# Kernel tuning notes

Measured on AMD Instinct MI355X. Metric: run time of the kernel, lower is better.

Reference implementation:

```python
import jax, jax.numpy as jnp
import numpy as np

# Mamba2 config (matches mamba_ssm.Mamba2 defaults used by the wrapper)
D_MODEL = 1024
D_STATE = 128
D_CONV = 4
EXPAND = 2
HEADDIM = 64
CHUNK = 256
D_INNER = EXPAND * D_MODEL            # 2048
NHEADS = D_INNER // HEADDIM           # 32
CONV_DIM = D_INNER + 2 * D_STATE      # 2304 (x, B, C share the causal conv)
D_IN_PROJ = 2 * D_INNER + 2 * D_STATE + NHEADS  # z, xBC, dt
EPS = 1e-5


def rmsnorm(x, w, eps=EPS):
    return x * jax.lax.rsqrt(jnp.mean(x * x, axis=-1, keepdims=True) + eps) * w


def setup_inputs() -> dict:
    key = jax.random.key(0)
    ks = jax.random.split(key, 8)
    B, L = 2, 2048
    def w(k, shape, sc=0.02):
        return jax.random.normal(k, shape, jnp.float32) * sc
    return {
        "x": jax.random.normal(ks[0], (B, L, D_MODEL), jnp.float32),
        "norm_w": jnp.ones((D_MODEL,), jnp.float32),
        "in_proj_w": w(ks[1], (D_IN_PROJ, D_MODEL)),
        "conv_w": w(ks[2], (CONV_DIM, 1, D_CONV), 0.2),   # depthwise kernel
        "conv_b": jnp.zeros((CONV_DIM,), jnp.float32),
        "dt_bias": w(ks[3], (NHEADS,), 1.0),
        "A_log": jnp.log(1.0 + 15.0 * jax.random.uniform(ks[4], (NHEADS,), jnp.float32)),
        "D": jnp.ones((NHEADS,), jnp.float32),
        "gnorm_w": jnp.ones((D_INNER,), jnp.float32),
        "out_proj_w": w(ks[5], (D_MODEL, D_INNER)),
    }


def _ssd(xd, a, Bm, Cm):
    """Chunked SSD scan (ssd_minimal_discrete).
    xd: (b,l,h,p) = x*dt ; a: (b,l,h) = dt*A ; Bm,Cm: (b,l,n) (ngroups=1)."""
    b, l, h, p = xd.shape
    n = Bm.shape[-1]
    nc = l // CHUNK
    xd = xd.reshape(b, nc, CHUNK, h, p)
    a = a.reshape(b, nc, CHUNK, h).transpose(0, 3, 1, 2)   # (b,h,nc,c)
    Bm = Bm.reshape(b, nc, CHUNK, n)
    Cm = Cm.reshape(b, nc, CHUNK, n)
    a_cs = jnp.cumsum(a, axis=-1)                           # (b,h,nc,c)
    # 1) intra-chunk: causal decay matrix L[t,s] = exp(sum_{s<i<=t} a_i)
    diff = a_cs[..., :, None] - a_cs[..., None, :]          # (b,h,nc,c,c)
    mask = jnp.tril(jnp.ones((CHUNK, CHUNK), bool))
    Lm = jnp.exp(jnp.where(mask, diff, 0.0)) * mask
    Y_diag = jnp.einsum("bcln,bcsn,bhcls,bcshp->bclhp", Cm, Bm, Lm, xd)
    # 2) per-chunk end states
    decay_states = jnp.exp(a_cs[..., -1:] - a_cs)           # (b,h,nc,c)
    states = jnp.einsum("bcln,bhcl,bclhp->bchpn", Bm, decay_states, xd)
    # 3) inter-chunk recurrence (vectorized segsum over the 8+1 chunk totals)
    tot = jnp.pad(a_cs[..., -1], ((0, 0), (0, 0), (1, 0)))  # (b,h,nc+1)
    tot_cs = jnp.cumsum(tot, axis=-1)
    dchunk = tot_cs[..., :, None] - tot_cs[..., None, :]    # (b,h,nc+1,nc+1)
    cmask = jnp.tril(jnp.ones((nc + 1, nc + 1), bool))
    dchunk = jnp.exp(jnp.where(cmask, dchunk, 0.0)) * cmask
    states = jnp.concatenate([jnp.zeros_like(states[:, :1]), states], axis=1)
    new_states = jnp.einsum("bhzc,bchpn->bzhpn", dchunk, states)
    init_states = new_states[:, :-1]                        # state entering each chunk
    # 4) state -> output contribution
    Y_off = jnp.einsum("bcln,bchpn,bhcl->bclhp", Cm, init_states, jnp.exp(a_cs))
    return (Y_diag + Y_off).reshape(b, l, h, p)


def reference(x, norm_w, in_proj_w, conv_w, conv_b, dt_bias, A_log, D, gnorm_w, out_proj_w):
    res = x
    u = rmsnorm(x, norm_w)
    zxbcdt = u @ in_proj_w.T                                # (b,l,d_in_proj)
    z, xBC, dt = jnp.split(zxbcdt, [D_INNER, D_INNER + CONV_DIM], axis=-1)
    # causal depthwise conv1d over (x,B,C), then SiLU
    xBC_t = jnp.pad(xBC.transpose(0, 2, 1), ((0, 0), (0, 0), (D_CONV - 1, 0)))
    conv = jax.lax.conv_general_dilated(
        xBC_t, conv_w, (1,), "VALID",
        dimension_numbers=("NCH", "OIH", "NCH"), feature_group_count=CONV_DIM)
    xBC = jax.nn.silu(conv.transpose(0, 2, 1) + conv_b)
    xs, Bm, Cm = jnp.split(xBC, [D_INNER, D_INNER + D_STATE], axis=-1)
    dt = jax.nn.softplus(dt + dt_bias)                      # (b,l,h)
    A = -jnp.exp(A_log)                                     # (h,)
    xh = xs.reshape(xs.shape[0], xs.shape[1], NHEADS, HEADDIM)
    y = _ssd(xh * dt[..., None], dt * A, Bm, Cm)
    y = y + D[None, None, :, None] * xh                     # skip term
    y = y.reshape(xs.shape)
    y = rmsnorm(y * jax.nn.silu(z), gnorm_w)                # gated RMSNorm
    return res + y @ out_proj_w.T
```

## Files before the change

kernel.cpp:

```cpp
#include <hip/hip_runtime.h>
#include <hip/hip_bf16.h>

typedef __hip_bfloat16 bf16_t;
typedef __attribute__((ext_vector_type(8))) short bfrag8;
typedef __attribute__((ext_vector_type(4))) float floatx4;

#define DM     1024
#define DI     2048
#define NHD    32
#define HD     64
#define DSTATE 128
#define CONVD  2304
#define NPROJ  4384
#define NPAD   4480
#define MR     4096
#define LL     2048
#define EPSF   1e-5f
#define LOG2E  1.44269504088896f

__device__ __forceinline__ void gl_lds16(const void* g, void* l) {
  __builtin_amdgcn_global_load_lds((const __attribute__((address_space(1))) void*)g,
                                   (__attribute__((address_space(3))) void*)l, 16, 0, 0);
}
__device__ __forceinline__ unsigned pack_bf16_rn(float a, float b) {
  unsigned ua = (__float_as_uint(a) + 0x8000u) >> 16;
  unsigned ub = (__float_as_uint(b) + 0x8000u) >> 16;
  return ua | (ub << 16);
}
__device__ __forceinline__ unsigned short bf16u(float a) {
  return (unsigned short)((__float_as_uint(a) + 0x8000u) >> 16);
}
__device__ __forceinline__ float blo(unsigned u){ return __uint_as_float(u << 16); }
__device__ __forceinline__ float bhi(unsigned u){ return __uint_as_float(u & 0xffff0000u); }
__device__ __forceinline__ void unp8(uint4 u, float* v) {
  v[0]=blo(u.x); v[1]=bhi(u.x); v[2]=blo(u.y); v[3]=bhi(u.y);
  v[4]=blo(u.z); v[5]=bhi(u.z); v[6]=blo(u.w); v[7]=bhi(u.w);
}
typedef union { unsigned u[4]; bfrag8 f; } fragu;

#define W1CNT (NPAD * DM / 4)
#define W2CNT (DM * DI / 4)
#define CVTBLK ((W1CNT + W2CNT) / 256)
__global__ void rms_cvt_kernel(const float* __restrict__ x, const float* __restrict__ w,
                               bf16_t* __restrict__ ub,
                               const float* __restrict__ w1, const float* __restrict__ w2,
                               const float* __restrict__ gw,
                               bf16_t* __restrict__ o1, bf16_t* __restrict__ o2) {
  __shared__ float red[4];
  int t = threadIdx.x;
  if (blockIdx.x < MR) {
    int row = blockIdx.x;
    float4 v = ((const float4*)(x + (long)row * DM))[t];
    float ss = v.x*v.x + v.y*v.y + v.z*v.z + v.w*v.w;
#pragma unroll
    for (int off = 32; off > 0; off >>= 1) ss += __shfl_down(ss, off, 64);
    if ((t & 63) == 0) red[t >> 6] = ss;
    __syncthreads();
    float tot = red[0] + red[1] + red[2] + red[3];
    float rs = rsqrtf(tot * (1.f / DM) + EPSF);
    float4 wv = ((const float4*)w)[t];
    bf16_t* o = ub + (long)row * DM + t * 4;
    o[0] = __float2bfloat16(v.x * rs * wv.x);
    o[1] = __float2bfloat16(v.y * rs * wv.y);
    o[2] = __float2bfloat16(v.z * rs * wv.z);
    o[3] = __float2bfloat16(v.w * rs * wv.w);
  } else {
    int i4 = (blockIdx.x - MR) * 256 + t;
    if (i4 < W1CNT) {
      int idx = i4 * 4;
      int row = idx >> 10;
      float4 v = make_float4(0.f, 0.f, 0.f, 0.f);
      if (row < NPROJ) v = *(const float4*)(w1 + idx);
      bf16_t* d = o1 + idx;
      d[0] = __float2bfloat16(v.x); d[1] = __float2bfloat16(v.y);
      d[2] = __float2bfloat16(v.z); d[3] = __float2bfloat16(v.w);
    } else {
      int idx = (i4 - W1CNT) * 4;
      int k = idx & (DI - 1);
      float4 v = *(const float4*)(w2 + idx);
      float4 g = *(const float4*)(gw + k);
      bf16_t* d = o2 + idx;
      d[0] = __float2bfloat16(v.x * g.x); d[1] = __float2bfloat16(v.y * g.y);
      d[2] = __float2bfloat16(v.z * g.z); d[3] = __float2bfloat16(v.w * g.w);
    }
  }
}

template<int TN, bool DO_RES, bool OUT_BF16>
__global__ __launch_bounds__(256) void gemm64_kernel(const bf16_t* __restrict__ A,
    const bf16_t* __restrict__ Bw, const float* __restrict__ resid,
    const float* __restrict__ ssqp, void* __restrict__ Cout, int N, int K) {
  __shared__ bf16_t As[128 * 64];
  __shared__ bf16_t Bs[TN * 64];
  __shared__ float rsS[128];
  const int tid = threadIdx.x;
  const int lane = tid & 63;
  const int wv = tid >> 6;
  const int l15 = lane & 15;
  const int l4 = lane >> 4;
  constexpr int MF = (TN == 128) ? 4 : 2;
  const int wm = (TN == 128) ? ((wv >> 1) << 6) : (wv << 5);
  const int wn = (TN == 128) ? ((wv & 1) << 6) : 0;
  const int tm = blockIdx.x << 7;
  const int tn = blockIdx.y * TN;

  if (DO_RES) {
    int rr = tid >> 1;
    const float4* pp = (const float4*)(ssqp + (long)(tm + rr) * 32 + (tid & 1) * 16);
    float s = 0.f;
#pragma unroll
    for (int q = 0; q < 4; q++) { float4 v = pp[q]; s += v.x + v.y + v.z + v.w; }
    s += __shfl_xor(s, 1, 64);
    if ((tid & 1) == 0) rsS[rr] = rsqrtf(s * (1.f / DI) + EPSF);
  }

  floatx4 acc[MF][4];
#pragma unroll
  for (int i = 0; i < MF; i++)
#pragma unroll
    for (int j = 0; j < 4; j++) acc[i][j] = (floatx4){0.f, 0.f, 0.f, 0.f};

  const int r = tid >> 3;
  const int c8 = tid & 7;
  const int scol = ((c8 ^ (r & 7)) << 3);
  const bf16_t* Ag = A + (long)(tm + r) * K + scol;
  const bf16_t* Bg = Bw + (long)(tn + r) * K + scol;
  const int swz = l15 & 7;

  for (int k0 = 0; k0 < K; k0 += 64) {
#pragma unroll
    for (int q = 0; q < 4; q++)
      gl_lds16(Ag + (long)(q * 32) * K + k0, &As[q * 2048 + tid * 8]);
#pragma unroll
    for (int q = 0; q < TN / 32; q++)
      gl_lds16(Bg + (long)(q * 32) * K + k0, &Bs[q * 2048 + tid * 8]);
    __syncthreads();
#pragma unroll
    for (int kk = 0; kk < 2; kk++) {
      bfrag8 af[MF], bfr[4];
      const int ch = ((kk << 2) | l4) ^ swz;
#pragma unroll
      for (int j = 0; j < 4; j++)
        bfr[j] = *(const bfrag8*)&Bs[(wn + j * 16 + l15) * 64 + ch * 8];
#pragma unroll
      for (int i = 0; i < MF; i++)
        af[i] = *(const bfrag8*)&As[(wm + i * 16 + l15) * 64 + ch * 8];
#pragma unroll
      for (int i = 0; i < MF; i++)
#pragma unroll
        for (int j = 0; j < 4; j++)
          acc[i][j] = __builtin_amdgcn_mfma_f32_16x16x32_bf16(af[i], bfr[j], acc[i][j], 0, 0, 0);
    }
    __syncthreads();
  }
#pragma unroll
  for (int i = 0; i < MF; i++)
#pragma unroll
    for (int j = 0; j < 4; j++)
#pragma unroll
      for (int r2 = 0; r2 < 4; r2++) {
        int row = tm + wm + i * 16 + l4 * 4 + r2;
        int col = tn + wn + j * 16 + l15;
        float v = acc[i][j][r2];
        if (OUT_BF16) {
          ((bf16_t*)Cout)[(long)row * N + col] = __float2bfloat16(v);
        } else {
          if (DO_RES) v = v * rsS[row - tm] + resid[(long)row * N + col];
          ((float*)Cout)[(long)row * N + col] = v;
        }
      }
}

__global__ __launch_bounds__(512, 2) void gemm256_kernel(const bf16_t* __restrict__ A,
    const bf16_t* __restrict__ Bw, bf16_t* __restrict__ Cout) {
  __shared__ bf16_t lds[65536];
  const int t = threadIdx.x;

  if (blockIdx.x >= 256) {
    const int idx = blockIdx.x - 256;
    const int mi = idx & 15, ni = idx >> 4;
    const int hh = t >> 8;
    const int tl = t & 255;
    const int lane = tl & 63, wv = tl >> 6;
    const int l15 = lane & 15, l4 = lane >> 4;
    const int wm = wv << 5;
    const int tm = mi * 256 + hh * 128;
    const int tn = 4096 + ni * 64;
    bf16_t* As = lds + hh * 8192;
    bf16_t* Bs = lds + 16384;
    floatx4 acc[2][4];
#pragma unroll
    for (int i = 0; i < 2; i++)
#pragma unroll
      for (int j = 0; j < 4; j++) acc[i][j] = (floatx4){0.f, 0.f, 0.f, 0.f};
    const int r = tl >> 3;
    const int c8 = tl & 7;
    const int scol = ((c8 ^ (r & 7)) << 3);
    const bf16_t* Ag = A + (long)(tm + r) * DM + scol;
    const bf16_t* Bg = Bw + (long)(tn + r) * DM + scol;
    const int swz = l15 & 7;
    for (int k0 = 0; k0 < DM; k0 += 64) {
#pragma unroll
      for (int q = 0; q < 4; q++)
        gl_lds16(Ag + (long)(q * 32) * DM + k0, &As[q * 2048 + tl * 8]);
      if (hh == 0) {
#pragma unroll
        for (int q = 0; q < 2; q++)
          gl_lds16(Bg + (long)(q * 32) * DM + k0, &Bs[q * 2048 + tl * 8]);
      }
      __syncthreads();
#pragma unroll
      for (int kk = 0; kk < 2; kk++) {
        bfrag8 af[2], bfr[4];
        const int ch = ((kk << 2) | l4) ^ swz;
#pragma unroll
        for (int j = 0; j < 4; j++)
          bfr[j] = *(const bfrag8*)&Bs[(j * 16 + l15) * 64 + ch * 8];
#pragma unroll
        for (int i = 0; i < 2; i++)
          af[i] = *(const bfrag8*)&As[(wm + i * 16 + l15) * 64 + ch * 8];
#pragma unroll
        for (int i = 0; i < 2; i++)
#pragma unroll
          for (int j = 0; j < 4; j++)
            acc[i][j] = __builtin_amdgcn_mfma_f32_16x16x32_bf16(af[i], bfr[j], acc[i][j], 0, 0, 0);
      }
      __syncthreads();
    }
#pragma unroll
    for (int i = 0; i < 2; i++)
#pragma unroll
      for (int j = 0; j < 4; j++)
#pragma unroll
        for (int r2 = 0; r2 < 4; r2++) {
          int row = tm + wm + i * 16 + l4 * 4 + r2;
          int col = tn + j * 16 + l15;
          Cout[(long)row * NPAD + col] = __float2bfloat16(acc[i][j][r2]);
        }
    return;
  }

  const int lane = t & 63, wv = t >> 6;
  const int wm = wv >> 2, wn = wv & 3;
  const int l15 = lane & 15, l4 = lane >> 4;
  const int xcd = blockIdx.x & 7, idx = blockIdx.x >> 3;
  const int bx = (xcd & 3) * 4 + (idx & 3);
  const int by = (xcd >> 2) * 8 + (idx >> 2);
  const int tm = bx << 8, tn = by << 8;

  const int srow = t >> 3;
  const int scol = ((t & 7) ^ (srow & 7)) << 3;
  const bf16_t* Ag = A + (long)(tm + srow) * DM + scol;
  const bf16_t* Bg = Bw + (long)(tn + srow) * DM + scol;
  bf16_t* Asl = lds;
  bf16_t* Bsl = lds + 32768;
  const int swl = (l15 & 7) << 4;
  const int ca0 = (l4 * 16) ^ swl;
  const int ca1 = (64 + l4 * 16) ^ swl;

  floatx4 acc[8][4];
#pragma unroll
  for (int i = 0; i < 8; i++)
#pragma unroll
    for (int j = 0; j < 4; j++) acc[i][j] = (floatx4){0.f, 0.f, 0.f, 0.f};
  bfrag8 bq[8];

#define STG_A(tt, h) { \
  bf16_t* d_ = Asl + (((tt) & 1) * 2 + (h)) * 8192 + t * 8; \
  gl_lds16(Ag + (long)((h) * 128     ) * DM + (tt) * 64, d_); \
  gl_lds16(Ag + (long)((h) * 128 + 64) * DM + (tt) * 64, d_ + 4096); \
}
#define STG_B(tt, h) { \
  bf16_t* d_ = Bsl + (((tt) & 1) * 2 + (h)) * 8192 + t * 8; \
  gl_lds16(Bg + (long)((h) * 128     ) * DM + (tt) * 64, d_); \
  gl_lds16(Bg + (long)((h) * 128 + 64) * DM + (tt) * 64, d_ + 4096); \
}
#define PH(d, q, STG, WT) { \
  const char* Ah_ = (const char*)(Asl + ((d) * 2 + wm) * 8192); \
  const char* Bh_ = (const char*)(Bsl + ((d) * 2 + (wn >> 1)) * 8192); \
  if ((q) == 0) { \
    _Pragma("unroll") \
    for (int j = 0; j < 4; j++) { \
      int r_ = ((wn & 1) << 6) + j * 16 + l15; \
      bq[j * 2]     = *(const bfrag8*)(Bh_ + r_ * 128 + ca0); \
      bq[j * 2 + 1] = *(const bfrag8*)(Bh_ + r_ * 128 + ca1); \
    } \
  } \
  bfrag8 aq0, aq1, aq2, aq3; \
  { int r_ = (q) * 32 + l15; \
    aq0 = *(const bfrag8*)(Ah_ + r_ * 128 + ca0); \
    aq1 = *(const bfrag8*)(Ah_ + r_ * 128 + ca1); \
    aq2 = *(const bfrag8*)(Ah_ + (r_ + 16) * 128 + ca0); \
    aq3 = *(const bfrag8*)(Ah_ + (r_ + 16) * 128 + ca1); } \
  STG; \
  __builtin_amdgcn_s_barrier(); \
  asm volatile("s_waitcnt lgkmcnt(0)" ::: "memory"); \
  __builtin_amdgcn_s_setprio(1); \
  _Pragma("unroll") \
  for (int j = 0; j < 4; j++) { \
    acc[(q)*2  ][j] = __builtin_amdgcn_mfma_f32_16x16x32_bf16(aq0, bq[j*2],   acc[(q)*2  ][j], 0, 0, 0); \
    acc[(q)*2  ][j] = __builtin_amdgcn_mfma_f32_16x16x32_bf16(aq1, bq[j*2+1], acc[(q)*2  ][j], 0, 0, 0); \
    acc[(q)*2+1][j] = __builtin_amdgcn_mfma_f32_16x16x32_bf16(aq2, bq[j*2],   acc[(q)*2+1][j], 0, 0, 0); \
    acc[(q)*2+1][j] = __builtin_amdgcn_mfma_f32_16x16x32_bf16(aq3, bq[j*2+1], acc[(q)*2+1][j], 0, 0, 0); \
  } \
  __builtin_amdgcn_s_setprio(0); \
  WT; \
  __builtin_amdgcn_s_barrier(); \
}

  STG_A(0, 0); STG_A(0, 1); STG_B(0, 0); STG_B(0, 1);
  STG_B(1, 0); STG_B(1, 1);
  asm volatile("s_waitcnt vmcnt(4)" ::: "memory");
  __builtin_amdgcn_s_barrier();

  for (int it = 0; it < 7; ++it) {
    const int ta = 2 * it, tb = ta + 1;
    PH(0, 0, STG_A(tb, 0), {})
    PH(0, 1, STG_A(tb, 1), {})
    PH(0, 2, STG_B(ta + 2, 0), {})
    PH(0, 3, STG_B(ta + 2, 1), asm volatile("s_waitcnt vmcnt(4)" ::: "memory");)
    PH(1, 0, STG_A(ta + 2, 0), {})
    PH(1, 1, STG_A(ta + 2, 1), {})
    PH(1, 2, STG_B(tb + 2, 0), {})
    PH(1, 3, STG_B(tb + 2, 1), asm volatile("s_waitcnt vmcnt(4)" ::: "memory");)
  }
  {
    PH(0, 0, STG_A(15, 0), {})
    PH(0, 1, STG_A(15, 1), {})
    PH(0, 2, {}, {})
    PH(0, 3, {}, asm volatile("s_waitcnt vmcnt(0)" ::: "memory");)
    PH(1, 0, {}, {})
    PH(1, 1, {}, {})
    PH(1, 2, {}, {})
    PH(1, 3, {}, {})
  }
#undef PH
#undef STG_A
#undef STG_B

  const long crow = tm + wm * 128;
  const int ccol = tn + wn * 64;
#pragma unroll
  for (int qi = 0; qi < 8; qi++)
#pragma unroll
    for (int j = 0; j < 4; j++)
#pragma unroll
      for (int r2 = 0; r2 < 4; r2++) {
        long row = crow + (qi >> 1) * 32 + (qi & 1) * 16 + l4 * 4 + r2;
        int col = ccol + j * 16 + l15;
        Cout[row * NPAD + col] = __float2bfloat16(acc[qi][j][r2]);
      }
}

__global__ __launch_bounds__(256) void sst_kernel(const bf16_t* __restrict__ xdTe,
    const bf16_t* __restrict__ BmT, bf16_t* __restrict__ states,
    const bf16_t* __restrict__ Cmh, const bf16_t* __restrict__ Bmh,
    bf16_t* __restrict__ SL) {
  __shared__ bf16_t As[128 * 32];
  __shared__ bf16_t Bs[128 * 32];
  const int t = threadIdx.x, lane = t & 63, wv = t >> 6;
  const int l15 = lane & 15, l4 = lane >> 4;
  if (blockIdx.x < 512) {
    int blk = blockIdx.x;
    int bc = blk >> 5;
    floatx4 acc[2][4];
#pragma unroll
    for (int i = 0; i < 2; i++)
#pragma unroll
      for (int j = 0; j < 4; j++) acc[i][j] = (floatx4){0.f, 0.f, 0.f, 0.f};
    const bf16_t* arow = BmT + (long)bc * 128 * 256;
    const bf16_t* brow = xdTe + (long)blk * 64 * 256;
#pragma unroll
    for (int kt = 0; kt < 8; kt++) {
      bfrag8 af[2], bfr[4];
#pragma unroll
      for (int i = 0; i < 2; i++)
        af[i] = *(const bfrag8*)(arow + (long)(wv * 32 + i * 16 + l15) * 256 + kt * 32 + l4 * 8);
#pragma unroll
      for (int j = 0; j < 4; j++)
        bfr[j] = *(const bfrag8*)(brow + (long)(j * 16 + l15) * 256 + kt * 32 + l4 * 8);
#pragma unroll
      for (int i = 0; i < 2; i++)
#pragma unroll
        for (int j = 0; j < 4; j++)
          acc[i][j] = __builtin_amdgcn_mfma_f32_16x16x32_bf16(af[i], bfr[j], acc[i][j], 0, 0, 0);
    }
#pragma unroll
    for (int i = 0; i < 2; i++)
#pragma unroll
      for (int j = 0; j < 4; j++) {
        int n_base = wv * 32 + i * 16 + l4 * 4;
        int p = j * 16 + l15;
        unsigned lo = pack_bf16_rn(acc[i][j][0], acc[i][j][1]);
        unsigned hi = pack_bf16_rn(acc[i][j][2], acc[i][j][3]);
        *(uint2*)(states + (long)blk * 8192 + p * 128 + n_base) = make_uint2(lo, hi);
      }
  } else {
    int idx = blockIdx.x - 512;
    const int bc = idx >> 2;
    const int tm = ((idx >> 1) & 1) << 7;
    const int tn = (idx & 1) << 7;
    const int wm = (wv >> 1) << 6;
    const int wn = (wv & 1) << 6;
    floatx4 acc[4][4];
#pragma unroll
    for (int i = 0; i < 4; i++)
#pragma unroll
      for (int j = 0; j < 4; j++) acc[i][j] = (floatx4){0.f, 0.f, 0.f, 0.f};
    const int arow = t >> 2;
    const int acol = (t & 3) << 3;
    const bf16_t* Ag = Cmh + (long)bc * 256 * DSTATE + (long)(tm + arow) * DSTATE + acol;
    const bf16_t* Bg = Bmh + (long)bc * 256 * DSTATE + (long)(tn + arow) * DSTATE + acol;
    const long k64 = (long)64 * DSTATE;
    for (int k0 = 0; k0 < DSTATE; k0 += 32) {
      gl_lds16(Ag + k0, &As[t * 8]);
      gl_lds16(Ag + k64 + k0, &As[2048 + t * 8]);
      gl_lds16(Bg + k0, &Bs[t * 8]);
      gl_lds16(Bg + k64 + k0, &Bs[2048 + t * 8]);
      __syncthreads();
      bfrag8 af[4], bfr[4];
#pragma unroll
      for (int i = 0; i < 4; i++)
        af[i] = *(const bfrag8*)&As[(wm + i * 16 + l15) * 32 + l4 * 8];
#pragma unroll
      for (int j = 0; j < 4; j++)
        bfr[j] = *(const bfrag8*)&Bs[(wn + j * 16 + l15) * 32 + l4 * 8];
#pragma unroll
      for (int i = 0; i < 4; i++)
#pragma unroll
        for (int j = 0; j < 4; j++)
          acc[i][j] = __builtin_amdgcn_mfma_f32_16x16x32_bf16(af[i], bfr[j], acc[i][j], 0, 0, 0);
      __syncthreads();
    }
    bf16_t* Cb = SL + (long)bc * 65536;
#pragma unroll
    for (int i = 0; i < 4; i++)
#pragma unroll
      for (int j = 0; j < 4; j++)
#pragma unroll
        for (int r = 0; r < 4; r++)
          Cb[(long)(tm + wm + i * 16 + l4 * 4 + r) * 256 + tn + wn + j * 16 + l15] =
              __float2bfloat16(acc[i][j][r]);
  }
}

__global__ __launch_bounds__(256) void conv4_kernel(const bf16_t* __restrict__ zxh,
    const float* __restrict__ cw, const float* __restrict__ cb,
    bf16_t* __restrict__ xhb, bf16_t* __restrict__ Bmh, bf16_t* __restrict__ Cmh) {
  int g = blockIdx.x * 256 + threadIdx.x;
  int cg = g % 288;
  int blt = g / 288;
  int c0 = cg * 8;
  long bl0 = (long)blt * 4;
  int l0 = (int)(bl0 & (LL - 1));
  const bf16_t* base = zxh + bl0 * NPAD + DI + c0;
  float rv[7][8];
#pragma unroll
  for (int j = 0; j < 7; j++) {
    int dj = j - 3;
    if (l0 + dj >= 0) {
      uint4 u = *(const uint4*)(base + (long)dj * NPAD);
      unp8(u, rv[j]);
    } else {
#pragma unroll
      for (int q = 0; q < 8; q++) rv[j][q] = 0.f;
    }
  }
  float4 wq[8];
#pragma unroll
  for (int q = 0; q < 8; q++) wq[q] = ((const float4*)cw)[c0 + q];
  float bias[8];
  *(float4*)&bias[0] = *(const float4*)(cb + c0);
  *(float4*)&bias[4] = *(const float4*)(cb + c0 + 4);
#pragma unroll
  for (int i = 0; i < 4; i++) {
    unsigned o[4];
#pragma unroll
    for (int q2 = 0; q2 < 4; q2++) {
      float rr[2];
#pragma unroll
      for (int e = 0; e < 2; e++) {
        int q = q2 * 2 + e;
        float a = bias[q] + wq[q].x * rv[i][q] + wq[q].y * rv[i + 1][q]
                + wq[q].z * rv[i + 2][q] + wq[q].w * rv[i + 3][q];
        rr[e] = a / (1.f + __expf(-a));
      }
      o[q2] = pack_bf16_rn(rr[0], rr[1]);
    }
    uint4 ov = make_uint4(o[0], o[1], o[2], o[3]);
    long bl = bl0 + i;
    if (c0 < DI)               *(uint4*)(xhb + bl * DI + c0) = ov;
    else if (c0 < DI + DSTATE) *(uint4*)(Bmh + bl * DSTATE + (c0 - DI)) = ov;
    else                       *(uint4*)(Cmh + bl * DSTATE + (c0 - DI - DSTATE)) = ov;
  }
}

__global__ __launch_bounds__(256) void xdt_kernel(const bf16_t* __restrict__ xhb,
    const bf16_t* __restrict__ Bmh, const bf16_t* __restrict__ zxh,
    const float* __restrict__ A_log, const float* __restrict__ dtb,
    float* __restrict__ acs, float* __restrict__ ctot,
    bf16_t* __restrict__ xdT, bf16_t* __restrict__ xdTe, bf16_t* __restrict__ BmT) {
  __shared__ unsigned short Tb[9216];
  __shared__ float acsL[256];
  __shared__ float dtsL[256];
  __shared__ float wsum[4];
  int blk = blockIdx.x;
  int t = threadIdx.x;
  if (blk < 512) {
    int h = blk & 31, bc = blk >> 5;
    {
      int lane = t & 63, w = t >> 6;
      float Ah = -__expf(A_log[h]) * LOG2E;
      int gl = bc * 256 + t;
      float vv = __bfloat162float(zxh[(long)gl * NPAD + (NPROJ - 32) + h]) + dtb[h];
      float sp = fmaxf(vv, 0.f) + log1pf(__expf(-fabsf(vv)));
      float a = sp * Ah;
#pragma unroll
      for (int off = 1; off < 64; off <<= 1) {
        float v = __shfl_up(a, off, 64);
        if (lane >= off) a += v;
      }
      if (lane == 63) wsum[w] = a;
      __syncthreads();
      float base = 0.f;
      for (int i = 0; i < 4; i++) base += (i < w) ? wsum[i] : 0.f;
      a += base;
      acsL[t] = a;
      dtsL[t] = sp;
      acs[blk * 256 + t] = a;
      if (t == 255) ctot[blk] = a;
      __syncthreads();
    }
    float atot = acsL[255];
    unsigned short* T1 = Tb;
    unsigned short* T2 = Tb + 4608;
    int l_loc = t >> 2, pg = t & 3;
    for (int lt = 0; lt < 4; lt++) {
      int ll = lt * 64 + l_loc;
      int gl = bc * 256 + ll;
      float w1 = dtsL[ll];
      float w2 = w1 * exp2f(atot - acsL[ll]);
      const uint4* src = (const uint4*)(xhb + (long)gl * DI + h * HD + pg * 16);
      uint4 u0 = src[0], u1 = src[1];
      float v[16];
      unp8(u0, v); unp8(u1, v + 8);
      __syncthreads();
#pragma unroll
      for (int q = 0; q < 16; q++) {
        T1[(pg * 16 + q) * 72 + l_loc] = bf16u(v[q] * w1);
        T2[(pg * 16 + q) * 72 + l_loc] = bf16u(v[q] * w2);
      }
      __syncthreads();
      long orow = ((long)blk * 64 + l_loc) * 256 + lt * 64 + pg * 16;
      *(uint4*)(xdT + orow)      = *(uint4*)&T1[l_loc * 72 + pg * 16];
      *(uint4*)(xdT + orow + 8)  = *(uint4*)&T1[l_loc * 72 + pg * 16 + 8];
      *(uint4*)(xdTe + orow)     = *(uint4*)&T2[l_loc * 72 + pg * 16];
      *(uint4*)(xdTe + orow + 8) = *(uint4*)&T2[l_loc * 72 + pg * 16 + 8];
    }
  } else {
    unsigned short* T = Tb;
    int bc = blk - 512;
    int l_loc = t >> 2, ng = t & 3;
    for (int lt = 0; lt < 4; lt++) {
      int gl = bc * 256 + lt * 64 + l_loc;
      const uint4* src = (const uint4*)(Bmh + (long)gl * DSTATE + ng * 32);
      uint4 u[4];
#pragma unroll
      for (int q = 0; q < 4; q++) u[q] = src[q];
      __syncthreads();
      const unsigned short* us = (const unsigned short*)u;
#pragma unroll
      for (int e = 0; e < 32; e++)
        T[(ng * 32 + e) * 72 + l_loc] = us[e];
      __syncthreads();
      int n = t >> 1, lg2 = t & 1;
      long orow = ((long)bc * 128 + n) * 256 + lt * 64 + lg2 * 32;
#pragma unroll
      for (int q = 0; q < 4; q++)
        *(uint4*)(BmT + orow + q * 8) = *(uint4*)&T[n * 72 + lg2 * 32 + q * 8];
    }
  }
}

__global__ void scan_kernel(const bf16_t* __restrict__ states, const float* __restrict__ ctot,
                            bf16_t* __restrict__ initsb) {
  int id = blockIdx.x * 256 + threadIdx.x;
  int pn = id & 8191;
  int bh = id >> 13;
  int b = bh >> 5, h = bh & 31;
  float S = 0.f;
#pragma unroll
  for (int c = 0; c < 8; c++) {
    int blk = (b * 8 + c) * 32 + h;
    initsb[(long)blk * 8192 + pn] = __float2bfloat16(S);
    S = exp2f(ctot[blk]) * S + __bfloat162float(states[(long)blk * 8192 + pn]);
  }
}

__global__ __launch_bounds__(512, 4) void yk4_kernel(const bf16_t* __restrict__ SL,
     const bf16_t* __restrict__ Cmh, const bf16_t* __restrict__ xhb,
     const bf16_t* __restrict__ zxh, const float* __restrict__ acs,
     const bf16_t* __restrict__ initsb, const bf16_t* __restrict__ xdT,
     const float* __restrict__ Dp, bf16_t* __restrict__ yg, float* __restrict__ ssqp) {
  int bi = blockIdx.x;
  int bc = (bi & 7) * 2 + ((bi >> 3) & 1);
  int h = bi >> 4;
  int ablk = bc * 32 + h;
  int t = threadIdx.x;
  int wv = t >> 6;
  int mh = wv >> 2, wsub = wv & 3;
  int lane = t & 63;
  int l15 = lane & 15, l4 = lane >> 4;

  __shared__ float acsS[256];
  __shared__ __align__(16) char bbuf[49152];
  bf16_t* xds = (bf16_t*)bbuf;
  bf16_t* ins = (bf16_t*)(bbuf + 32768);
  float* Yt = (float*)bbuf;

  {
    const bf16_t* xrow_g = xdT + (long)ablk * 64 * 256;
#pragma unroll
    for (int it = 0; it < 4; it++) {
      int sl = it * 512 + t;
      int p = sl >> 5, s = sl & 31;
      int c = (s & 24) | ((s & 7) ^ (p & 7));
      gl_lds16(xrow_g + p * 256 + c * 8, &xds[sl * 8]);
    }
    const bf16_t* irow_g = initsb + (long)ablk * 8192;
#pragma unroll
    for (int it = 0; it < 2; it++) {
      int sl = it * 512 + t;
      int p = sl >> 4, s = sl & 15;
      int c = (s & 8) | ((s & 7) ^ (p & 7));
      gl_lds16(irow_g + p * 128 + c * 8, &ins[sl * 8]);
    }
  }
  if (t < 256) acsS[t] = acs[ablk * 256 + t];
  __syncthreads();

  const int rowbase = bc * 256;
  const int l0 = mh * 128 + wsub * 32 + l15;
  const int l1 = l0 + 16;
  const float al0 = acsS[l0], al1 = acsS[l1];
  const float eA0 = exp2f(al0), eA1 = exp2f(al1);
  const bf16_t* SL0 = SL + (long)bc * 65536 + (long)l0 * 256;
  const bf16_t* SL1 = SL + (long)bc * 65536 + (long)l1 * 256;

  floatx4 acc[2][4];
#pragma unroll
  for (int i = 0; i < 2; i++)
#pragma unroll
    for (int j = 0; j < 4; j++) acc[i][j] = (floatx4){0.f, 0.f, 0.f, 0.f};

  const int nkd = (mh + 1) * 4;
  for (int kt = 0; kt < nkd; kt++) {
    int sbase = kt * 32 + l4 * 8;
    float as[8];
    *(float4*)&as[0] = *(const float4*)&acsS[sbase];
    *(float4*)&as[4] = *(const float4*)&acsS[sbase + 4];
    float sv0[8], sv1[8];
    unp8(*(const uint4*)(SL0 + sbase), sv0);
    unp8(*(const uint4*)(SL1 + sbase), sv1);
    fragu af0, af1;
#pragma unroll
    for (int q2 = 0; q2 < 4; q2++) {
      float p00, p01, p10, p11;
      {
        int s = sbase + q2 * 2;
        float d0 = al0 - as[q2 * 2], d1 = al0 - as[q2 * 2 + 1];
        p00 = (s <= l0) ? sv0[q2 * 2] * exp2f(fminf(d0, 0.f)) : 0.f;
        p01 = (s + 1 <= l0) ? sv0[q2 * 2 + 1] * exp2f(fminf(d1, 0.f)) : 0.f;
        float e0 = al1 - as[q2 * 2], e1 = al1 - as[q2 * 2 + 1];
        p10 = (s <= l1) ? sv1[q2 * 2] * exp2f(fminf(e0, 0.f)) : 0.f;
        p11 = (s + 1 <= l1) ? sv1[q2 * 2 + 1] * exp2f(fminf(e1, 0.f)) : 0.f;
      }
      af0.u[q2] = pack_bf16_rn(p00, p01);
      af1.u[q2] = pack_bf16_rn(p10, p11);
    }
    bfrag8 bfr[4];
    int ch = kt * 4 + l4;
#pragma unroll
    for (int j = 0; j < 4; j++) {
      int p = j * 16 + l15;
      int sw = (ch & 24) | ((ch & 7) ^ (p & 7));
      bfr[j] = *(const bfrag8*)&xds[(p * 32 + sw) * 8];
    }
#pragma unroll
    for (int j = 0; j < 4; j++) {
      acc[0][j] = __builtin_amdgcn_mfma_f32_16x16x32_bf16(af0.f, bfr[j], acc[0][j], 0, 0, 0);
      acc[1][j] = __builtin_amdgcn_mfma_f32_16x16x32_bf16(af1.f, bfr[j], acc[1][j], 0, 0, 0);
    }
  }
#pragma unroll
  for (int kt = 0; kt < 4; kt++) {
    int n0 = kt * 32 + l4 * 8;
    uint4 c0 = *(const uint4*)(Cmh + (long)(rowbase + l0) * DSTATE + n0);
    uint4 c1 = *(const uint4*)(Cmh + (long)(rowbase + l1) * DSTATE + n0);
    float cv0[8], cv1[8];
    unp8(c0, cv0); unp8(c1, cv1);
    fragu af0, af1;
#pragma unroll
    for (int q2 = 0; q2 < 4; q2++) {
      af0.u[q2] = pack_bf16_rn(cv0[q2 * 2] * eA0, cv0[q2 * 2 + 1] * eA0);
      af1.u[q2] = pack_bf16_rn(cv1[q2 * 2] * eA1, cv1[q2 * 2 + 1] * eA1);
    }
    bfrag8 bfr[4];
    int ch = kt * 4 + l4;
#pragma unroll
    for (int j = 0; j < 4; j++) {
      int p = j * 16 + l15;
      int sw = (ch & 8) | ((ch & 7) ^ (p & 7));
      bfr[j] = *(const bfrag8*)&ins[(p * 16 + sw) * 8];
    }
#pragma unroll
    for (int j = 0; j < 4; j++) {
      acc[0][j] = __builtin_amdgcn_mfma_f32_16x16x32_bf16(af0.f, bfr[j], acc[0][j], 0, 0, 0);
      acc[1][j] = __builtin_amdgcn_mfma_f32_16x16x32_bf16(af1.f, bfr[j], acc[1][j], 0, 0, 0);
    }
  }
  float Dh = Dp[h];
#pragma unroll
  for (int pass = 0; pass < 2; pass++) {
    __syncthreads();
    if (mh == pass) {
#pragma unroll
      for (int i = 0; i < 2; i++)
#pragma unroll
        for (int j = 0; j < 4; j++)
#pragma unroll
          for (int r = 0; r < 4; r++)
            Yt[(wsub * 32 + i * 16 + l4 * 4 + r) * 66 + j * 16 + l15] = acc[i][j][r];
    }
    __syncthreads();
    {
      int row_l = t >> 2;
      int chc = (t & 3) * 16;
      long rowg = rowbase + pass * 128 + row_l;
      float ss = 0.f;
#pragma unroll
      for (int it = 0; it < 2; it++) {
        int c = chc + it * 8;
        float4 y0 = *(const float4*)&Yt[row_l * 66 + c];
        float4 y1 = *(const float4*)&Yt[row_l * 66 + c + 4];
        uint4 ux = *(const uint4*)(xhb + rowg * DI + h * HD + c);
        uint4 uz = *(const uint4*)(zxh + rowg * NPAD + h * HD + c);
        float xv[8], zv[8];
        unp8(ux, xv); unp8(uz, zv);
        float yv[8] = {y0.x, y0.y, y0.z, y0.w, y1.x, y1.y, y1.z, y1.w};
        unsigned o[4];
#pragma unroll
        for (int q = 0; q < 4; q++) {
          float v0 = (yv[q * 2 + 0] + Dh * xv[q * 2 + 0]) *
                     (zv[q * 2 + 0] / (1.f + __expf(-zv[q * 2 + 0])));
          float v1 = (yv[q * 2 + 1] + Dh * xv[q * 2 + 1]) *
                     (zv[q * 2 + 1] / (1.f + __expf(-zv[q * 2 + 1])));
          ss += v0 * v0 + v1 * v1;
          o[q] = pack_bf16_rn(v0, v1);
        }
        *(uint4*)(yg + rowg * DI + h * HD + c) = make_uint4(o[0], o[1], o[2], o[3]);
      }
      ss += __shfl_xor(ss, 1, 64);
      ss += __shfl_xor(ss, 2, 64);
      if ((t & 3) == 0) ssqp[rowg * 32 + h] = ss;
    }
  }
}

extern "C" void kernel_launch(void* const* d_in, const int* in_sizes, int n_in,
                              void* d_out, int out_size, void* d_ws, size_t ws_size,
                              hipStream_t stream) {
  const float* x    = (const float*)d_in[0];
  const float* nw   = (const float*)d_in[1];
  const float* w1   = (const float*)d_in[2];
  const float* cw   = (const float*)d_in[3];
  const float* cb   = (const float*)d_in[4];
  const float* dtb  = (const float*)d_in[5];
  const float* alog = (const float*)d_in[6];
  const float* Dp   = (const float*)d_in[7];
  const float* gw   = (const float*)d_in[8];
  const float* w2   = (const float*)d_in[9];
  float* out = (float*)d_out;

  char* ws = (char*)d_ws;
  size_t off = 0;
  auto alloc = [&](size_t bytes) -> void* {
    void* p = ws + off;
    off += (bytes + 255) & ~(size_t)255;
    return p;
  };
  bf16_t* ub     = (bf16_t*)alloc((size_t)MR * DM * 2);
  bf16_t* w1b    = (bf16_t*)alloc((size_t)NPAD * DM * 2);
  bf16_t* w2b    = (bf16_t*)alloc((size_t)DM * DI * 2);
  bf16_t* zxh    = (bf16_t*)alloc((size_t)MR * NPAD * 2);
  bf16_t* xhb    = (bf16_t*)alloc((size_t)MR * DI * 2);
  bf16_t* Bmh    = (bf16_t*)alloc((size_t)MR * DSTATE * 2);
  bf16_t* Cmh    = (bf16_t*)alloc((size_t)MR * DSTATE * 2);
  bf16_t* SL     = (bf16_t*)alloc((size_t)16 * 256 * 256 * 2);
  float* acs     = (float*)alloc((size_t)512 * 256 * 4);
  float* ctot    = (float*)alloc((size_t)512 * 4);
  bf16_t* states = (bf16_t*)alloc((size_t)512 * 8192 * 2);
  bf16_t* initsb = (bf16_t*)alloc((size_t)512 * 8192 * 2);
  bf16_t* xdT    = (bf16_t*)alloc((size_t)512 * 64 * 256 * 2);
  bf16_t* xdTe   = (bf16_t*)alloc((size_t)512 * 64 * 256 * 2);
  bf16_t* BmT    = (bf16_t*)alloc((size_t)16 * 128 * 256 * 2);
  bf16_t* yg     = (bf16_t*)alloc((size_t)MR * DI * 2);
  float* ssqp    = (float*)alloc((size_t)MR * NHD * 4);
  if (off > ws_size) return;

  rms_cvt_kernel<<<MR + CVTBLK, 256, 0, stream>>>(x, nw, ub, w1, w2, gw, w1b, w2b);
  gemm256_kernel<<<352, 512, 0, stream>>>(ub, w1b, zxh);
  conv4_kernel<<<(1024 * 288) / 256, 256, 0, stream>>>(zxh, cw, cb, xhb, Bmh, Cmh);
  xdt_kernel<<<528, 256, 0, stream>>>(xhb, Bmh, zxh, alog, dtb, acs, ctot, xdT, xdTe, BmT);
  sst_kernel<<<576, 256, 0, stream>>>(xdTe, BmT, states, Cmh, Bmh, SL);
  scan_kernel<<<(2 * 32 * 8192) / 256, 256, 0, stream>>>(states, ctot, initsb);
  yk4_kernel<<<512, 512, 0, stream>>>(SL, Cmh, xhb, zxh, acs, initsb, xdT, Dp, yg, ssqp);
  gemm64_kernel<64, true, false><<<dim3(MR / 128, DM / 64), 256, 0, stream>>>(
      yg, w2b, x, ssqp, out, DM, DI);
}
```

Before: 250.5 us.

## Double-buffer GEMM tail blocks, drop padded tail tiles, XCD-swizzle out-proj GEMM

The N-tail blocks of the in-projection GEMM now double-buffer their LDS tiles. The next k-slice is issued with global_load_lds before the current one is computed, synchronised with explicit vmcnt waits and barriers, and B is loaded by all 512 threads at once. The grid shrinks from 352 to 336 blocks, so one fully padded 64-column tail strip beyond NPROJ is no longer computed. The output-projection GEMM remaps block indices so that blocks sharing an XCD work on neighbouring M/N tiles, aiming for better L2 reuse. The cost is twice the LDS use in the tail path and hand-written waitcnt sequencing, which is fragile.

```diff
diff --git a/kernel.cpp b/kernel.cpp
--- a/kernel.cpp
+++ b/kernel.cpp
@@ -101,8 +101,16 @@
   constexpr int MF = (TN == 128) ? 4 : 2;
   const int wm = (TN == 128) ? ((wv >> 1) << 6) : (wv << 5);
   const int wn = (TN == 128) ? ((wv & 1) << 6) : 0;
-  const int tm = blockIdx.x << 7;
-  const int tn = blockIdx.y * TN;
+  int tm, tn;
+  if (DO_RES) {
+    const int flat = blockIdx.y * gridDim.x + blockIdx.x;
+    const int xcd = flat & 7, ridx = flat >> 3;
+    tm = ((xcd & 3) * 8 + (ridx & 7)) << 7;
+    tn = ((xcd >> 2) * 8 + (ridx >> 3)) * TN;
+  } else {
+    tm = blockIdx.x << 7;
+    tn = blockIdx.y * TN;
+  }
 
   if (DO_RES) {
     int rr = tid >> 1;
@@ -186,47 +194,60 @@
     const int wm = wv << 5;
     const int tm = mi * 256 + hh * 128;
     const int tn = 4096 + ni * 64;
-    bf16_t* As = lds + hh * 8192;
-    bf16_t* Bs = lds + 16384;
+    bf16_t* As = lds + hh * 16384;
+    bf16_t* Bs = lds + 32768;
     floatx4 acc[2][4];
 #pragma unroll
     for (int i = 0; i < 2; i++)
 #pragma unroll
       for (int j = 0; j < 4; j++) acc[i][j] = (floatx4){0.f, 0.f, 0.f, 0.f};
-    const int r = tl >> 3;
-    const int c8 = tl & 7;
+    const int r = tl >> 3, c8 = tl & 7;
     const int scol = ((c8 ^ (r & 7)) << 3);
     const bf16_t* Ag = A + (long)(tm + r) * DM + scol;
-    const bf16_t* Bg = Bw + (long)(tn + r) * DM + scol;
+    const int rb = t >> 3, cb8 = t & 7;
+    const int sbcol = ((cb8 ^ (rb & 7)) << 3);
+    const bf16_t* Bg = Bw + (long)(tn + rb) * DM + sbcol;
     const int swz = l15 & 7;
-    for (int k0 = 0; k0 < DM; k0 += 64) {
-#pragma unroll
-      for (int q = 0; q < 4; q++)
-        gl_lds16(Ag + (long)(q * 32) * DM + k0, &As[q * 2048 + tl * 8]);
-      if (hh == 0) {
-#pragma unroll
-        for (int q = 0; q < 2; q++)
-          gl_lds16(Bg + (long)(q * 32) * DM + k0, &Bs[q * 2048 + tl * 8]);
-      }
-      __syncthreads();
+
+#define RSTG(k) { \
+    const int bb_ = (k) & 1; \
+    _Pragma("unroll") \
+    for (int q = 0; q < 4; q++) \
+      gl_lds16(Ag + (long)(q * 32) * DM + (k) * 64, &As[bb_ * 8192 + q * 2048 + tl * 8]); \
+    gl_lds16(Bg + (k) * 64, &Bs[bb_ * 4096 + t * 8]); \
+}
+    RSTG(0)
+    for (int k = 0; k < 16; k++) {
+      if (k < 15) {
+        RSTG(k + 1)
+        asm volatile("s_waitcnt vmcnt(5)" ::: "memory");
+      } else {
+        asm volatile("s_waitcnt vmcnt(0)" ::: "memory");
+      }
+      __builtin_amdgcn_s_barrier();
+      asm volatile("" ::: "memory");
+      const int bb = k & 1;
 #pragma unroll
       for (int kk = 0; kk < 2; kk++) {
         bfrag8 af[2], bfr[4];
         const int ch = ((kk << 2) | l4) ^ swz;
 #pragma unroll
         for (int j = 0; j < 4; j++)
-          bfr[j] = *(const bfrag8*)&Bs[(j * 16 + l15) * 64 + ch * 8];
+          bfr[j] = *(const bfrag8*)&Bs[bb * 4096 + (j * 16 + l15) * 64 + ch * 8];
 #pragma unroll
         for (int i = 0; i < 2; i++)
-          af[i] = *(const bfrag8*)&As[(wm + i * 16 + l15) * 64 + ch * 8];
+          af[i] = *(const bfrag8*)&As[bb * 8192 + (wm + i * 16 + l15) * 64 + ch * 8];
 #pragma unroll
         for (int i = 0; i < 2; i++)
 #pragma unroll
           for (int j = 0; j < 4; j++)
             acc[i][j] = __builtin_amdgcn_mfma_f32_16x16x32_bf16(af[i], bfr[j], acc[i][j], 0, 0, 0);
       }
-      __syncthreads();
-    }
+      asm volatile("" ::: "memory");
+      __builtin_amdgcn_s_barrier();
+      asm volatile("" ::: "memory");
+    }
+#undef RSTG
 #pragma unroll
     for (int i = 0; i < 2; i++)
 #pragma unroll
@@ -809,7 +830,7 @@
   if (off > ws_size) return;
 
   rms_cvt_kernel<<<MR + CVTBLK, 256, 0, stream>>>(x, nw, ub, w1, w2, gw, w1b, w2b);
-  gemm256_kernel<<<352, 512, 0, stream>>>(ub, w1b, zxh);
+  gemm256_kernel<<<336, 512, 0, stream>>>(ub, w1b, zxh);
   conv4_kernel<<<(1024 * 288) / 256, 256, 0, stream>>>(zxh, cw, cb, xhb, Bmh, Cmh);
   xdt_kernel<<<528, 256, 0, stream>>>(xhb, Bmh, zxh, alog, dtb, acs, ctot, xdT, xdTe, BmT);
   sst_kernel<<<576, 256, 0, stream>>>(xdTe, BmT, states, Cmh, Bmh, SL);
```

New measurement: 249.3 us. About the same (-0.5%).
